# Performance work log

Hardware: AMD Instinct MI355X
Metric: run time of the kernel (lower is better)

The kernel has to match this reference:

```python
import jax, jax.numpy as jnp
import numpy as np

N, E, B = 50000, 800000, 1000
NODE_DIN, BB_DOUT, DHID, K = 32, 64, 64, 3
GLOB_DIN, EMBED_DIN = 64, 64
CIN = BB_DOUT + NODE_DIN  # 96


def setup_inputs() -> dict:
    key = jax.random.key(0)
    ks = jax.random.split(key, 24)

    def w(k, shape, fan_in):
        return jax.random.normal(k, shape, jnp.float32) / np.float32(np.sqrt(fan_in))

    inp = dict(
        x=jax.random.normal(ks[0], (N, NODE_DIN), jnp.float32),
        u=jax.random.normal(ks[1], (B, GLOB_DIN), jnp.float32),
        z=jax.random.normal(ks[2], (N, BB_DOUT), jnp.float32),
        edge_index=jax.random.randint(ks[3], (2, E), 0, N),
        edge_weight=jax.random.uniform(ks[4], (E,), jnp.float32),
        batch=jnp.sort(jax.random.randint(ks[5], (N,), 0, B)),
        batch_size=B,
        prev_h=jax.random.normal(ks[6], (N, DHID), jnp.float32),
    )
    # six ChebConvs of GConvGRU: x-convs take CIN, h-convs take DHID; all output DHID
    for i, nm in enumerate(["xz", "hz", "xr", "hr", "xh", "hh"]):
        cin = CIN if nm[0] == "x" else DHID
        inp[f"W{nm}"] = w(ks[7 + 2 * i], (K, cin, DHID), cin * K)
        inp[f"b{nm}"] = jnp.zeros((DHID,), jnp.float32)
    inp["Wg"] = w(ks[20], (GLOB_DIN, EMBED_DIN), GLOB_DIN)
    inp["bg"] = jnp.zeros((EMBED_DIN,), jnp.float32)
    return inp


def _cheb(xin, W, b, src, dst, w_norm, n):
    """ChebConv with sym norm, lambda_max=2 -> L_hat = -D^-1/2 A D^-1/2 (diag cancels)."""
    def prop(t):  # L_hat @ t  ([N,C])
        return -jax.ops.segment_sum(w_norm[:, None] * t[src], dst, num_segments=n)

    out = xin @ W[0] + b
    tx_prev = xin
    tx = None
    if W.shape[0] > 1:
        tx = prop(xin)
        out = out + tx @ W[1]
    for k in range(2, W.shape[0]):
        tx_new = 2.0 * prop(tx) - tx_prev
        out = out + tx_new @ W[k]
        tx_prev, tx = tx, tx_new
    return out


def reference(x, u, z, edge_index, edge_weight, batch, batch_size, prev_h,
              Wxz, bxz, Whz, bhz, Wxr, bxr, Whr, bhr, Wxh, bxh, Whh, bhh, Wg, bg):
    n = x.shape[0]
    src, dst = edge_index[0], edge_index[1]
    deg = jax.ops.segment_sum(edge_weight, src, num_segments=n)
    deg_safe = jnp.where(deg > 0, deg, 1.0)
    dinv = jnp.where(deg > 0, jax.lax.rsqrt(deg_safe), 0.0)
    w_norm = dinv[src] * edge_weight * dinv[dst]

    xin = jnp.concatenate([z, x], axis=-1)  # [N, CIN]
    Z = jax.nn.sigmoid(_cheb(xin, Wxz, bxz, src, dst, w_norm, n)
                       + _cheb(prev_h, Whz, bhz, src, dst, w_norm, n))
    R = jax.nn.sigmoid(_cheb(xin, Wxr, bxr, src, dst, w_norm, n)
                       + _cheb(prev_h, Whr, bhr, src, dst, w_norm, n))
    Ht = jnp.tanh(_cheb(xin, Wxh, bxh, src, dst, w_norm, n)
                  + _cheb(prev_h * R, Whh, bhh, src, dst, w_norm, n))
    h = Z * prev_h + (1.0 - Z) * Ht

    graph_emb = jax.ops.segment_sum(z, batch, num_segments=batch_size)  # [B, BB_DOUT]
    global_emb = jax.nn.relu(u @ Wg + bg)                                # [B, EMBED_DIN]
    fused = jnp.concatenate([graph_emb, global_emb], axis=-1)           # [B, 128]
    return fused, h
```

## Files before the change

kernel.cpp:

```cpp
#include <hip/hip_runtime.h>

#define NN 50000
#define EE 800000
#define BB 1000
#define NB 196
#define NCOPY 8

typedef unsigned short u16;
typedef __attribute__((ext_vector_type(8))) short bf16x8;
typedef __attribute__((ext_vector_type(4))) float f32x4;

static __device__ __forceinline__ u16 f2b(float f) {
    union { float f; unsigned u; } v;
    v.f = f;
    unsigned r = v.u + 0x7fffu + ((v.u >> 16) & 1u);
    return (u16)(r >> 16);
}

static __device__ __forceinline__ float b2f(short s) {
    union { unsigned u; float f; } c;
    c.u = ((unsigned)(u16)s) << 16;
    return c.f;
}

__global__ void k_degcnt(const int* __restrict__ src, const int* __restrict__ dst,
                         const float* __restrict__ ew, float* __restrict__ deg_p,
                         int* __restrict__ cnt_p) {
    int e = blockIdx.x * 256 + threadIdx.x;
    if (e >= EE) return;
    int cp = blockIdx.x & (NCOPY - 1);
    atomicAdd(&deg_p[(size_t)cp * NN + src[e]], ew[e]);
    atomicAdd(&cnt_p[(size_t)cp * NN + dst[e]], 1);
}

__global__ void k_scan1(const int* __restrict__ cnt_p, int* __restrict__ cnt,
                        int* __restrict__ incl, int* __restrict__ bsum) {
    __shared__ int s[256];
    int i = blockIdx.x * 256 + threadIdx.x;
    int v = 0;
    if (i < NN) {
#pragma unroll
        for (int p = 0; p < NCOPY; p++) v += cnt_p[(size_t)p * NN + i];
        cnt[i] = v;
    }
    s[threadIdx.x] = v;
    __syncthreads();
    for (int off = 1; off < 256; off <<= 1) {
        int t = (threadIdx.x >= off) ? s[threadIdx.x - off] : 0;
        __syncthreads();
        s[threadIdx.x] += t;
        __syncthreads();
    }
    if (i < NN) incl[i] = s[threadIdx.x];
    if (threadIdx.x == 255) bsum[blockIdx.x] = s[255];
}

__global__ void k_scan2(int* __restrict__ bsum) {
    __shared__ int s[256];
    int v = (threadIdx.x < NB) ? bsum[threadIdx.x] : 0;
    s[threadIdx.x] = v;
    __syncthreads();
    for (int off = 1; off < 256; off <<= 1) {
        int t = (threadIdx.x >= off) ? s[threadIdx.x - off] : 0;
        __syncthreads();
        s[threadIdx.x] += t;
        __syncthreads();
    }
    if (threadIdx.x < NB) bsum[threadIdx.x] = s[threadIdx.x];
}

__global__ void k_scan3(const int* __restrict__ incl, const int* __restrict__ cnt,
                        const int* __restrict__ bsum, int* __restrict__ row_ptr,
                        int* __restrict__ cursor, const float* __restrict__ deg_p,
                        float* __restrict__ dinv) {
    int i = blockIdx.x * 256 + threadIdx.x;
    if (i >= NN) return;
    int off = (blockIdx.x > 0) ? bsum[blockIdx.x - 1] : 0;
    int start = off + incl[i] - cnt[i];
    row_ptr[i] = start;
    cursor[i] = start;
    float d = 0.f;
#pragma unroll
    for (int p = 0; p < NCOPY; p++) d += deg_p[(size_t)p * NN + i];
    dinv[i] = d > 0.f ? rsqrtf(d) : 0.f;
}

__global__ void k_scatter(const int* __restrict__ src, const int* __restrict__ dst,
                          const float* __restrict__ ew, const float* __restrict__ dinv,
                          int* __restrict__ cursor, uint2* __restrict__ csr8) {
    int e = blockIdx.x * 256 + threadIdx.x;
    if (e >= EE) return;
    int d = dst[e], s = src[e];
    int pos = atomicAdd(&cursor[d], 1);
    float w = dinv[s] * ew[e] * dinv[d];
    csr8[pos] = make_uint2((unsigned)s, __float_as_uint(w));
}

__global__ void k_build_A(const float* __restrict__ z, const float* __restrict__ x,
                          const float* __restrict__ ph, u16* __restrict__ A) {
    int i = blockIdx.x * 256 + threadIdx.x;
    if (i >= NN * 160) return;
    int n = i / 160, c = i - n * 160;
    float v;
    if (c < 64) v = z[n * 64 + c];
    else if (c < 96) v = x[n * 32 + (c - 64)];
    else v = ph[n * 64 + (c - 96)];
    A[(size_t)n * 480 + c] = f2b(v);
}

__global__ void k_packW_all(const float* __restrict__ Wxz, const float* __restrict__ Wxr,
                            const float* __restrict__ Wxh, const float* __restrict__ Whz,
                            const float* __restrict__ Whr, const float* __restrict__ Whh,
                            u16* __restrict__ Wp, u16* __restrict__ W3p) {
    int idx = blockIdx.x * 256 + threadIdx.x;
    if (idx < 15 * 12 * 512) {
        int j = idx & 7, l = (idx >> 3) & 63;
        int ct = (idx >> 9) % 12, s = (idx >> 9) / 12;
        int k = 32 * s + (l >> 4) * 8 + j;
        int g = ct >> 2;
        int c = 16 * (ct & 3) + (l & 15);
        bool isX;
        int kr;
        if (k < 96)       { isX = true;  kr = k; }
        else if (k < 160) { isX = false; kr = k - 96; }
        else if (k < 256) { isX = true;  kr = 96 + (k - 160); }
        else if (k < 320) { isX = false; kr = 64 + (k - 256); }
        else if (k < 416) { isX = true;  kr = 192 + (k - 320); }
        else              { isX = false; kr = 128 + (k - 416); }
        float val;
        if (isX) {
            const float* W = (g == 0) ? Wxz : ((g == 1) ? Wxr : Wxh);
            val = W[kr * 64 + c];
        } else if (g == 2) {
            val = 0.f;
        } else {
            const float* W = (g == 0) ? Whz : Whr;
            val = W[kr * 64 + c];
        }
        Wp[idx] = f2b(val);
    } else {
        int i2 = idx - 15 * 12 * 512;
        if (i2 >= 6 * 4 * 512) return;
        int j = i2 & 7, l = (i2 >> 3) & 63;
        int ct = (i2 >> 9) & 3, s = i2 >> 11;
        int k = 32 * s + (l >> 4) * 8 + j;
        int ki = k >> 6, kr = k & 63;
        int c = 16 * ct + (l & 15);
        W3p[i2] = f2b(Whh[(ki * 64 + kr) * 64 + c]);
    }
}

template <int C, int SCALE, bool HB, int BS, int OS>
__global__ __launch_bounds__(BS) void k_pull(
    const u16* __restrict__ Abase, int inofs, int baseofs, int outofs,
    const uint2* __restrict__ csr8, const int* __restrict__ row_ptr,
    const int* __restrict__ cnt) {
    constexpr int TPR = C / 8;
    int tid = blockIdx.x * BS + threadIdx.x;
    int r = tid / TPR;
    int c8 = (tid - r * TPR) * 8;
    if (r >= NN) return;
    int s0 = row_ptr[r], n = cnt[r];
    float acc[8] = {0.f, 0.f, 0.f, 0.f, 0.f, 0.f, 0.f, 0.f};
    const u16* in = Abase + inofs + c8;
    uint2 e = (n > 0) ? csr8[s0] : make_uint2(0u, 0u);
    for (int j = 0; j < n; j++) {
        uint2 ec = e;
        if (j + 1 < n) e = csr8[s0 + j + 1];
        float w = __uint_as_float(ec.y);
        bf16x8 v = *(const bf16x8*)(in + (size_t)ec.x * OS);
#pragma unroll
        for (int k = 0; k < 8; k++) acc[k] += w * b2f(v[k]);
    }
    const float sc = -(float)SCALE;
    float o[8];
    if (HB) {
        bf16x8 b = *(const bf16x8*)(Abase + (size_t)r * OS + baseofs + c8);
#pragma unroll
        for (int k = 0; k < 8; k++) o[k] = sc * acc[k] - b2f(b[k]);
    } else {
#pragma unroll
        for (int k = 0; k < 8; k++) o[k] = sc * acc[k];
    }
    bf16x8 p;
#pragma unroll
    for (int k = 0; k < 8; k++) p[k] = (short)f2b(o[k]);
    *(bf16x8*)(const_cast<u16*>(Abase) + (size_t)r * OS + outofs + c8) = p;
}

__global__ __launch_bounds__(256) void k_gates_mfma(
    const u16* __restrict__ A, const u16* __restrict__ Wp,
    const float* __restrict__ bxz, const float* __restrict__ bhz,
    const float* __restrict__ bxr, const float* __restrict__ bhr,
    const float* __restrict__ bxh,
    u16* __restrict__ Zb16, u16* __restrict__ Hx16, u16* __restrict__ A3) {
    int wv = (blockIdx.x * 256 + threadIdx.x) >> 6;
    int lane = threadIdx.x & 63;
    int r0 = wv * 16;
    if (r0 >= NN) return;
    int q = lane >> 4, j0 = lane & 15;

    f32x4 acc[12];
#pragma unroll
    for (int i = 0; i < 12; i++) acc[i] = (f32x4){0.f, 0.f, 0.f, 0.f};

    const u16* arow = A + (size_t)(r0 + j0) * 480 + q * 8;
#pragma unroll
    for (int s = 0; s < 15; s++) {
        bf16x8 a = *(const bf16x8*)(arow + 32 * s);
        const u16* bp = Wp + (size_t)(s * 12) * 512 + lane * 8;
#pragma unroll
        for (int ct = 0; ct < 12; ct++) {
            bf16x8 b = *(const bf16x8*)(bp + ct * 512);
            acc[ct] = __builtin_amdgcn_mfma_f32_16x16x32_bf16(a, b, acc[ct], 0, 0, 0);
        }
    }

#pragma unroll
    for (int ct = 0; ct < 4; ct++) {
        int j = 16 * ct + j0;
        float bz = bxz[j] + bhz[j];
        float br = bxr[j] + bhr[j];
        float bh = bxh[j];
#pragma unroll
        for (int reg = 0; reg < 4; reg++) {
            int r = r0 + q * 4 + reg;
            size_t i = (size_t)r * 64 + j;
            float zp = acc[ct][reg] + bz;
            float rp = acc[ct + 4][reg] + br;
            float hp = acc[ct + 8][reg] + bh;
            float zv = 1.f / (1.f + expf(-zp));
            float rv = 1.f / (1.f + expf(-rp));
            float phv = b2f((short)A[(size_t)r * 480 + 96 + j]);
            Zb16[i] = f2b(zv);
            Hx16[i] = f2b(hp);
            A3[(size_t)r * 192 + j] = f2b(rv * phv);
        }
    }
}

__global__ __launch_bounds__(256) void k_final_mfma(
    const u16* __restrict__ A3, const u16* __restrict__ W3p,
    const float* __restrict__ bhh, const u16* __restrict__ Hx16,
    const u16* __restrict__ Zb16, const u16* __restrict__ A,
    float* __restrict__ outh) {
    int wv = (blockIdx.x * 256 + threadIdx.x) >> 6;
    int lane = threadIdx.x & 63;
    int r0 = wv * 16;
    if (r0 >= NN) return;
    int q = lane >> 4, j0 = lane & 15;

    f32x4 acc[4];
#pragma unroll
    for (int i = 0; i < 4; i++) acc[i] = (f32x4){0.f, 0.f, 0.f, 0.f};

    const u16* arow = A3 + (size_t)(r0 + j0) * 192 + q * 8;
#pragma unroll
    for (int s = 0; s < 6; s++) {
        bf16x8 a = *(const bf16x8*)(arow + 32 * s);
        const u16* bp = W3p + (size_t)(s * 4) * 512 + lane * 8;
#pragma unroll
        for (int ct = 0; ct < 4; ct++) {
            bf16x8 b = *(const bf16x8*)(bp + ct * 512);
            acc[ct] = __builtin_amdgcn_mfma_f32_16x16x32_bf16(a, b, acc[ct], 0, 0, 0);
        }
    }

#pragma unroll
    for (int ct = 0; ct < 4; ct++) {
        int j = 16 * ct + j0;
        float bh = bhh[j];
#pragma unroll
        for (int reg = 0; reg < 4; reg++) {
            int r = r0 + q * 4 + reg;
            size_t i = (size_t)r * 64 + j;
            float ht = tanhf(b2f((short)Hx16[i]) + acc[ct][reg] + bh);
            float zv = b2f((short)Zb16[i]);
            float phv = b2f((short)A[(size_t)r * 480 + 96 + j]);
            outh[i] = zv * phv + (1.f - zv) * ht;
        }
    }
}

__global__ void k_gemb(const float* __restrict__ z, const int* __restrict__ batch,
                       float* __restrict__ gemb) {
    int wave = (blockIdx.x * 256 + threadIdx.x) >> 6;
    int lane = threadIdx.x & 63;
    int n0 = wave * 64;
    if (n0 >= NN) return;
    int nend = n0 + 64 < NN ? n0 + 64 : NN;
    float acc = 0.f;
    int cur = batch[n0];
    for (int n = n0; n < nend; n++) {
        int b = batch[n];
        if (b != cur) {
            atomicAdd(&gemb[(size_t)cur * 64 + lane], acc);
            acc = 0.f;
            cur = b;
        }
        acc += z[(size_t)n * 64 + lane];
    }
    atomicAdd(&gemb[(size_t)cur * 64 + lane], acc);
}

__global__ __launch_bounds__(256) void k_fused(
    const float* __restrict__ u, const float* __restrict__ Wg, const float* __restrict__ bg,
    const float* __restrict__ gemb, float* __restrict__ out) {
    int t = blockIdx.x * 256 + threadIdx.x;
    int r = t >> 6, c = t & 63;
    if (r >= BB) return;
    float acc = bg[c];
    const float* ur = u + (size_t)r * 64;
    for (int k = 0; k < 64; k++) acc += ur[k] * Wg[k * 64 + c];
    acc = fmaxf(acc, 0.f);
    out[(size_t)r * 128 + c] = gemb[(size_t)r * 64 + c];
    out[(size_t)r * 128 + 64 + c] = acc;
}

extern "C" void kernel_launch(void* const* d_in, const int* in_sizes, int n_in,
                              void* d_out, int out_size, void* d_ws, size_t ws_size,
                              hipStream_t stream) {
    const float* x  = (const float*)d_in[0];
    const float* u  = (const float*)d_in[1];
    const float* z  = (const float*)d_in[2];
    const int*   ei = (const int*)d_in[3];
    const float* ew = (const float*)d_in[4];
    const int* batch = (const int*)d_in[5];
    const float* ph = (const float*)d_in[7];
    const float *Wxz = (const float*)d_in[8],  *bxz = (const float*)d_in[9];
    const float *Whz = (const float*)d_in[10], *bhz = (const float*)d_in[11];
    const float *Wxr = (const float*)d_in[12], *bxr = (const float*)d_in[13];
    const float *Whr = (const float*)d_in[14], *bhr = (const float*)d_in[15];
    const float *Wxh = (const float*)d_in[16], *bxh = (const float*)d_in[17];
    const float *Whh = (const float*)d_in[18], *bhh = (const float*)d_in[19];
    const float *Wg  = (const float*)d_in[20], *bg  = (const float*)d_in[21];
    const int* src = ei;
    const int* dst = ei + EE;

    char* wsb = (char*)d_ws;
    size_t o = 0;
    auto alloc = [&](size_t bytes) {
        void* p = wsb + o;
        o += (bytes + 255) & ~(size_t)255;
        return p;
    };
    float* deg_p   = (float*)alloc((size_t)NCOPY * NN * 4);
    int*   cnt_p   = (int*)alloc((size_t)NCOPY * NN * 4);
    int*   cnt     = (int*)alloc(NN * 4);
    int*   incl    = (int*)alloc(NN * 4);
    int*   row_ptr = (int*)alloc(NN * 4);
    int*   cursor  = (int*)alloc(NN * 4);
    float* dinv    = (float*)alloc(NN * 4);
    int*   bsum    = (int*)alloc(256 * 4);
    uint2* csr8    = (uint2*)alloc((size_t)EE * 8);
    u16*   Zb16 = (u16*)alloc((size_t)NN * 64 * 2);
    u16*   Hx16 = (u16*)alloc((size_t)NN * 64 * 2);
    float* gemb = (float*)alloc((size_t)BB * 64 * 4);
    u16*   A    = (u16*)alloc((size_t)NN * 480 * 2);
    u16*   A3   = (u16*)alloc((size_t)NN * 192 * 2);
    u16*   Wp   = (u16*)alloc(15 * 12 * 512 * 2);
    u16*   W3p  = (u16*)alloc(6 * 4 * 512 * 2);

    float* outF = (float*)d_out;
    float* outH = outF + (size_t)BB * 128;

    const int BLK = 256;
    const int gE = (EE + BLK - 1) / BLK;
    const int gA = (NN * 160 + BLK - 1) / BLK;
    const int gPull160 = (NN + 15) / 16;
    const int gPull64 = (NN + 31) / 32;
    const int gMFMA = (3125 + 3) / 4;
    const int gPack = (15 * 12 * 512 + 6 * 4 * 512 + BLK - 1) / BLK;

    k_packW_all<<<gPack, BLK, 0, stream>>>(Wxz, Wxr, Wxh, Whz, Whr, Whh, Wp, W3p);
    k_build_A<<<gA, BLK, 0, stream>>>(z, x, ph, A);

    hipMemsetAsync(deg_p, 0, (size_t)2 * NCOPY * NN * 4, stream);
    k_degcnt<<<gE, BLK, 0, stream>>>(src, dst, ew, deg_p, cnt_p);

    k_scan1<<<NB, 256, 0, stream>>>(cnt_p, cnt, incl, bsum);
    k_scan2<<<1, 256, 0, stream>>>(bsum);
    k_scan3<<<NB, 256, 0, stream>>>(incl, cnt, bsum, row_ptr, cursor, deg_p, dinv);
    k_scatter<<<gE, BLK, 0, stream>>>(src, dst, ew, dinv, cursor, csr8);

    k_pull<160, 1, false, 320, 480><<<gPull160, 320, 0, stream>>>(A, 0, 0, 160, csr8, row_ptr, cnt);
    k_pull<160, 2, true, 320, 480><<<gPull160, 320, 0, stream>>>(A, 160, 0, 320, csr8, row_ptr, cnt);

    k_gates_mfma<<<gMFMA, BLK, 0, stream>>>(A, Wp, bxz, bhz, bxr, bhr, bxh, Zb16, Hx16, A3);

    k_pull<64, 1, false, 256, 192><<<gPull64, 256, 0, stream>>>(A3, 0, 0, 64, csr8, row_ptr, cnt);
    k_pull<64, 2, true, 256, 192><<<gPull64, 256, 0, stream>>>(A3, 64, 0, 128, csr8, row_ptr, cnt);

    k_final_mfma<<<gMFMA, BLK, 0, stream>>>(A3, W3p, bhh, Hx16, Zb16, A, outH);

    hipMemsetAsync(gemb, 0, (size_t)BB * 64 * 4, stream);
    k_gemb<<<(NN + BLK - 1) / BLK, BLK, 0, stream>>>(z, batch, gemb);
    k_fused<<<(BB * 64 + BLK - 1) / BLK, BLK, 0, stream>>>(u, Wg, bg, gemb, outF);
}
```

Before: 455.5 us.

## Build degree and count histograms in LDS and fuse graph-embedding tail

Replaces the global-atomic degree/count kernel with a range-partitioned LDS histogram. Each block owns a node range and an edge chunk, accumulates with shared-memory atomics, and writes a per-chunk partial with plain stores, so the memset is no longer needed. The scans now reduce 32 partials instead of 8. The graph-embedding segment sum and global-embedding MLP are fused into one kernel that uses binary search on the sorted batch array, removing the atomics, a memset and a launch. In exchange, every edge chunk is read 8 times (once per node range), and the partial arrays and their reduction are larger.

```diff
diff --git a/kernel.cpp b/kernel.cpp
--- a/kernel.cpp
+++ b/kernel.cpp
@@ -4,7 +4,10 @@
 #define EE 800000
 #define BB 1000
 #define NB 196
-#define NCOPY 8
+#define NR 8
+#define RS 6272
+#define NC 32
+#define CHUNK 25000
 
 typedef unsigned short u16;
 typedef __attribute__((ext_vector_type(8))) short bf16x8;
@@ -23,14 +26,34 @@
     return c.f;
 }
 
-__global__ void k_degcnt(const int* __restrict__ src, const int* __restrict__ dst,
-                         const float* __restrict__ ew, float* __restrict__ deg_p,
-                         int* __restrict__ cnt_p) {
-    int e = blockIdx.x * 256 + threadIdx.x;
-    if (e >= EE) return;
-    int cp = blockIdx.x & (NCOPY - 1);
-    atomicAdd(&deg_p[(size_t)cp * NN + src[e]], ew[e]);
-    atomicAdd(&cnt_p[(size_t)cp * NN + dst[e]], 1);
+__global__ __launch_bounds__(512) void k_degcnt_lds(
+    const int* __restrict__ src, const int* __restrict__ dst,
+    const float* __restrict__ ew, float* __restrict__ deg_p,
+    int* __restrict__ cnt_p) {
+    __shared__ float sdeg[RS];
+    __shared__ int scnt[RS];
+    int r = blockIdx.x & (NR - 1);
+    int c = blockIdx.x >> 3;
+    int base = r * RS;
+    for (int i = threadIdx.x; i < RS; i += 512) {
+        sdeg[i] = 0.f;
+        scnt[i] = 0;
+    }
+    __syncthreads();
+    int e0 = c * CHUNK;
+    for (int j = threadIdx.x; j < CHUNK; j += 512) {
+        int e = e0 + j;
+        int s = src[e], d = dst[e];
+        int sl = s - base, dl = d - base;
+        if ((unsigned)sl < RS) atomicAdd(&sdeg[sl], ew[e]);
+        if ((unsigned)dl < RS) atomicAdd(&scnt[dl], 1);
+    }
+    __syncthreads();
+    int lim = (NN - base < RS) ? (NN - base) : RS;
+    for (int i = threadIdx.x; i < lim; i += 512) {
+        deg_p[(size_t)c * NN + base + i] = sdeg[i];
+        cnt_p[(size_t)c * NN + base + i] = scnt[i];
+    }
 }
 
 __global__ void k_scan1(const int* __restrict__ cnt_p, int* __restrict__ cnt,
@@ -40,7 +63,7 @@
     int v = 0;
     if (i < NN) {
 #pragma unroll
-        for (int p = 0; p < NCOPY; p++) v += cnt_p[(size_t)p * NN + i];
+        for (int p = 0; p < NC; p++) v += cnt_p[(size_t)p * NN + i];
         cnt[i] = v;
     }
     s[threadIdx.x] = v;
@@ -81,7 +104,7 @@
     cursor[i] = start;
     float d = 0.f;
 #pragma unroll
-    for (int p = 0; p < NCOPY; p++) d += deg_p[(size_t)p * NN + i];
+    for (int p = 0; p < NC; p++) d += deg_p[(size_t)p * NN + i];
     dinv[i] = d > 0.f ? rsqrtf(d) : 0.f;
 }
 
@@ -282,39 +305,33 @@
     }
 }
 
-__global__ void k_gemb(const float* __restrict__ z, const int* __restrict__ batch,
-                       float* __restrict__ gemb) {
-    int wave = (blockIdx.x * 256 + threadIdx.x) >> 6;
+__global__ __launch_bounds__(256) void k_tail(
+    const float* __restrict__ z, const int* __restrict__ batch,
+    const float* __restrict__ u, const float* __restrict__ Wg,
+    const float* __restrict__ bg, float* __restrict__ out) {
+    int b = (blockIdx.x * 256 + threadIdx.x) >> 6;
     int lane = threadIdx.x & 63;
-    int n0 = wave * 64;
-    if (n0 >= NN) return;
-    int nend = n0 + 64 < NN ? n0 + 64 : NN;
+    if (b >= BB) return;
+    int lo = 0, hi = NN;
+    while (lo < hi) {
+        int m = (lo + hi) >> 1;
+        if (batch[m] < b) lo = m + 1; else hi = m;
+    }
+    int start = lo;
+    hi = NN;
+    while (lo < hi) {
+        int m = (lo + hi) >> 1;
+        if (batch[m] < b + 1) lo = m + 1; else hi = m;
+    }
+    int end = lo;
     float acc = 0.f;
-    int cur = batch[n0];
-    for (int n = n0; n < nend; n++) {
-        int b = batch[n];
-        if (b != cur) {
-            atomicAdd(&gemb[(size_t)cur * 64 + lane], acc);
-            acc = 0.f;
-            cur = b;
-        }
-        acc += z[(size_t)n * 64 + lane];
-    }
-    atomicAdd(&gemb[(size_t)cur * 64 + lane], acc);
-}
-
-__global__ __launch_bounds__(256) void k_fused(
-    const float* __restrict__ u, const float* __restrict__ Wg, const float* __restrict__ bg,
-    const float* __restrict__ gemb, float* __restrict__ out) {
-    int t = blockIdx.x * 256 + threadIdx.x;
-    int r = t >> 6, c = t & 63;
-    if (r >= BB) return;
-    float acc = bg[c];
-    const float* ur = u + (size_t)r * 64;
-    for (int k = 0; k < 64; k++) acc += ur[k] * Wg[k * 64 + c];
-    acc = fmaxf(acc, 0.f);
-    out[(size_t)r * 128 + c] = gemb[(size_t)r * 64 + c];
-    out[(size_t)r * 128 + 64 + c] = acc;
+    for (int n = start; n < end; n++) acc += z[(size_t)n * 64 + lane];
+    float g = bg[lane];
+    const float* ur = u + (size_t)b * 64;
+    for (int k = 0; k < 64; k++) g += ur[k] * Wg[k * 64 + lane];
+    g = fmaxf(g, 0.f);
+    out[(size_t)b * 128 + lane] = acc;
+    out[(size_t)b * 128 + 64 + lane] = g;
 }
 
 extern "C" void kernel_launch(void* const* d_in, const int* in_sizes, int n_in,
@@ -344,8 +361,8 @@
         o += (bytes + 255) & ~(size_t)255;
         return p;
     };
-    float* deg_p   = (float*)alloc((size_t)NCOPY * NN * 4);
-    int*   cnt_p   = (int*)alloc((size_t)NCOPY * NN * 4);
+    float* deg_p   = (float*)alloc((size_t)NC * NN * 4);
+    int*   cnt_p   = (int*)alloc((size_t)NC * NN * 4);
     int*   cnt     = (int*)alloc(NN * 4);
     int*   incl    = (int*)alloc(NN * 4);
     int*   row_ptr = (int*)alloc(NN * 4);
@@ -355,7 +372,6 @@
     uint2* csr8    = (uint2*)alloc((size_t)EE * 8);
     u16*   Zb16 = (u16*)alloc((size_t)NN * 64 * 2);
     u16*   Hx16 = (u16*)alloc((size_t)NN * 64 * 2);
-    float* gemb = (float*)alloc((size_t)BB * 64 * 4);
     u16*   A    = (u16*)alloc((size_t)NN * 480 * 2);
     u16*   A3   = (u16*)alloc((size_t)NN * 192 * 2);
     u16*   Wp   = (u16*)alloc(15 * 12 * 512 * 2);
@@ -375,8 +391,7 @@
     k_packW_all<<<gPack, BLK, 0, stream>>>(Wxz, Wxr, Wxh, Whz, Whr, Whh, Wp, W3p);
     k_build_A<<<gA, BLK, 0, stream>>>(z, x, ph, A);
 
-    hipMemsetAsync(deg_p, 0, (size_t)2 * NCOPY * NN * 4, stream);
-    k_degcnt<<<gE, BLK, 0, stream>>>(src, dst, ew, deg_p, cnt_p);
+    k_degcnt_lds<<<NR * NC, 512, 0, stream>>>(src, dst, ew, deg_p, cnt_p);
 
     k_scan1<<<NB, 256, 0, stream>>>(cnt_p, cnt, incl, bsum);
     k_scan2<<<1, 256, 0, stream>>>(bsum);
@@ -393,7 +408,5 @@
 
     k_final_mfma<<<gMFMA, BLK, 0, stream>>>(A3, W3p, bhh, Hx16, Zb16, A, outH);
 
-    hipMemsetAsync(gemb, 0, (size_t)BB * 64 * 4, stream);
-    k_gemb<<<(NN + BLK - 1) / BLK, BLK, 0, stream>>>(z, batch, gemb);
-    k_fused<<<(BB * 64 + BLK - 1) / BLK, BLK, 0, stream>>>(u, Wg, bg, gemb, outF);
-}
+    k_tail<<<(BB * 64 + BLK - 1) / BLK, BLK, 0, stream>>>(z, batch, u, Wg, bg, outF);
+}
```

Result: faster. 425.7 us (-6.5%).
